# Kernel tuning notes

Hardware: AMD Instinct MI355X
Metric: run time of the kernel (lower is better)

## Reference

```python
import jax, jax.numpy as jnp
import numpy as np

# --- model hyperparams (match init_kwargs) ---
N_DIM = 200      # n_dim == nfeat == nhidden (Linear(200,200) hardcoded in source)
NHID = 200
NLAYERS = 8
ALPHA = 0.1
LAMDA = 0.5
B, L = 20, 100   # dialogues x uniform dialogue length
N = B * L        # 2000 utterances per modality -> 3N = 6000 graph nodes
A_DIM, V_DIM, L_DIM, NSPK = 300, 342, 1024, 2


def _linear_params(key, fin, fout):
    s = 1.0 / np.sqrt(fin)
    k1, k2 = jax.random.split(key)
    W = jax.random.uniform(k1, (fin, fout), jnp.float32, -s, s)
    b = jax.random.uniform(k2, (fout,), jnp.float32, -s, s)
    return W, b


def setup_inputs() -> dict:
    key = jax.random.key(0)
    ks = jax.random.split(key, 12)
    a = jax.random.normal(ks[0], (N, A_DIM), jnp.float32)
    v = jax.random.normal(ks[1], (N, V_DIM), jnp.float32)
    l = jax.random.normal(ks[2], (N, L_DIM), jnp.float32)
    qmask = jax.random.uniform(ks[3], (L, B, NSPK), dtype=jnp.float32)
    # dense normalized adjacency over the 3N-node multimodal graph
    adj = jax.random.uniform(ks[4], (3 * N, 3 * N), dtype=jnp.float32) / (3.0 * N)
    Wa, ba = _linear_params(ks[5], A_DIM, N_DIM)
    Wv, bv = _linear_params(ks[6], V_DIM, N_DIM)
    Wl, bl = _linear_params(ks[7], L_DIM, N_DIM)
    spk_emb = jax.random.normal(ks[8], (NSPK, N_DIM), jnp.float32)
    W0, b0 = _linear_params(ks[9], N_DIM, NHID)
    s = 1.0 / np.sqrt(NHID)
    # variant=True -> conv weight is [2*nhidden, nhidden]
    convW = jax.random.uniform(ks[10], (NLAYERS, 2 * NHID, NHID), jnp.float32, -s, s)
    return dict(a=a, v=v, l=l, qmask=qmask, adj=adj,
                Wa=Wa, ba=ba, Wv=Wv, bv=bv, Wl=Wl, bl=bl,
                spk_emb=spk_emb, W0=W0, b0=b0, convW=convW, dia_len=L)


def reference(a, v, l, qmask, adj, Wa, ba, Wv, bv, Wl, bl, spk_emb, W0, b0, convW, dia_len):
    # modality projections
    a = a @ Wa + ba                                   # [N, n_dim]
    v = v @ Wv + bv
    l = l @ Wl + bl
    # qmask: [L, B, n_spk] seq-first -> concat per dialogue (uniform lengths)
    qcat = jnp.transpose(qmask[:dia_len], (1, 0, 2)).reshape(-1, qmask.shape[-1])  # [N, n_spk]
    spk_idx = jnp.argmax(qcat, axis=-1)
    l = l + spk_emb[spk_idx]                          # use_speaker, 'l' in modals
    # big multimodal graph: stack modalities along node axis
    x = jnp.concatenate([a, v, l], axis=0)            # [3N, n_dim]
    # GCNII_lyc (eval mode: dropout identity)
    h0 = jax.nn.relu(x @ W0 + b0)                     # [3N, nhidden]
    thetas = jnp.log(LAMDA / jnp.arange(1, NLAYERS + 1, dtype=jnp.float32) + 1.0)

    def layer(h, wt):
        W, theta = wt
        hi = adj @ h                                  # spmm (dense here)
        support = jnp.concatenate([hi, h0], axis=1)   # variant=True
        r = (1.0 - ALPHA) * hi + ALPHA * h0
        h_new = jax.nn.relu(theta * (support @ W) + (1.0 - theta) * r)
        return h_new, None

    h, _ = jax.lax.scan(layer, h0, (convW, thetas))
    feat = jnp.concatenate([x, h], axis=1)            # use_residue -> [3N, n_dim+nhidden]
    n = a.shape[0]
    # split modality chunks back and fuse on feature axis -> [N, 3*(n_dim+nhidden)]
    return jnp.concatenate([feat[:n], feat[n:2 * n], feat[2 * n:3 * n]], axis=-1)
```

## Files before the change

### kernel.cpp

```cpp
#include <hip/hip_runtime.h>
#include <math.h>

typedef unsigned short u16;
typedef unsigned int u32;
typedef __bf16 bf8_t __attribute__((ext_vector_type(8)));
typedef float f4_t __attribute__((ext_vector_type(4)));
typedef u16 us8_t __attribute__((ext_vector_type(8)));
typedef u16 us4_t __attribute__((ext_vector_type(4)));

#define LDC 224
#define NROWS 6016
#define PLANE (NROWS*LDC)

__device__ __forceinline__ float b2f(u16 x){
  union{u32 u; float f;} c; c.u = ((u32)x)<<16; return c.f;
}
__device__ __forceinline__ u16 f2b(float f){
  union{u32 u; float f;} c; c.f = f;
  u32 b = c.u;
  return (u16)((b + 0x7FFFu + ((b>>16)&1u)) >> 16);
}
__device__ __forceinline__ u16 ldcvt(const void* p, size_t i, int f){
  return f ? f2b(((const float*)p)[i]) : ((const u16*)p)[i];
}
__device__ __forceinline__ void gl16(const u16* g, u16* l){
  __builtin_amdgcn_global_load_lds((const __attribute__((address_space(1))) void*)g,
                                   (__attribute__((address_space(3))) void*)l, 16, 0, 0);
}

__global__ void detect_kernel(const u16* __restrict__ adj, int* __restrict__ flag)
{
  int l = threadIdx.x;
  u16 u = adj[2*l];
  int ex = (u >> 7) & 0xFF;
  bool ok = ((u >> 15) == 0) && (ex >= 0x30) && (ex <= 0x72);
  unsigned long long m = __ballot(ok);
  if (l == 0) flag[0] = (__popcll(m) < 32) ? 1 : 0;
}

#define PB_MISC 5320
#define PB_XPAD 5333
#define PB_AP   5347
#define PB_VP   7907
#define PB_CONV 10979
__global__ void prep_kernel(const int* __restrict__ flag,
                            const void* __restrict__ adj, u16* __restrict__ adj_bf,
                            const void* __restrict__ Wa, const void* __restrict__ Wv,
                            const void* __restrict__ Wl, const void* __restrict__ W0,
                            const void* __restrict__ convW, const void* __restrict__ qmask,
                            const void* __restrict__ a_in, const void* __restrict__ v_in,
                            const void* __restrict__ spkemb_in,
                            const void* __restrict__ ba, const void* __restrict__ bv,
                            const void* __restrict__ bl, const void* __restrict__ b0,
                            u16* __restrict__ WaT, u16* __restrict__ WvT, u16* __restrict__ WlT,
                            u16* __restrict__ W0T, u16* __restrict__ WtT, u16* __restrict__ WbT,
                            int* __restrict__ spk, u16* __restrict__ x_bf,
                            u16* __restrict__ a_p, u16* __restrict__ v_p,
                            u16* __restrict__ spkem, u16* __restrict__ b_all)
{
  const int f = flag[0];
  const int bid = blockIdx.x;
  const int tid = threadIdx.x;

  if (bid < PB_MISC){
    u32 e = (u32)bid*256u + (u32)tid;
    const void* src; u16* dst; u32 K, kpad; u32 soff = 0;
    if (e < 71680u){ src=Wa; dst=WaT; K=300; kpad=320; }
    else if (e < 157696u){ e -= 71680u;  src=Wv; dst=WvT; K=342; kpad=384; }
    else if (e < 387072u){ e -= 157696u; src=Wl; dst=WlT; K=1024; kpad=1024; }
    else if (e < 444416u){ e -= 387072u; src=W0; dst=W0T; K=200; kpad=256; }
    else if (e < 903168u){ e -= 444416u; u32 i = e/57344u; e -= i*57344u;
                           src=convW; soff=i*80000u;          dst=WtT + i*57344; K=200; kpad=256; }
    else {                 e -= 903168u; u32 i = e/57344u; e -= i*57344u;
                           src=convW; soff=i*80000u + 40000u; dst=WbT + i*57344; K=200; kpad=256; }
    u32 k = e / 224u, n = e - k*224u;
    u16 val = 0;
    if (k < K && n < 200u) val = ldcvt(src, (size_t)soff + (size_t)k*200u + n, f);
    dst[(size_t)n*kpad + k] = val;
    return;
  }
  if (bid < PB_XPAD){
    int e = (bid - PB_MISC)*256 + tid;
    if (e < 2000){
      int b = e/100, t = e - b*100;
      size_t base = ((size_t)t*20 + b)*2;
      bool one;
      if (f) one = ((const float*)qmask)[base+1] > ((const float*)qmask)[base];
      else   one = b2f(((const u16*)qmask)[base+1]) > b2f(((const u16*)qmask)[base]);
      spk[e] = one ? 1 : 0;
    } else if (e < 2400){
      spkem[e-2000] = ldcvt(spkemb_in, e-2000, f);
    } else if (e < 3200){
      int j = e - 2400; int which = j/200, idx = j - which*200;
      const void* src = (which==0)?ba:(which==1)?bv:(which==2)?bl:b0;
      b_all[j] = ldcvt(src, idx, f);
    }
    return;
  }
  if (bid < PB_AP){
    int e = (bid - PB_XPAD)*256 + tid;
    if (e < 16*LDC) x_bf[(size_t)6000*LDC + e] = 0;
    return;
  }
  if (bid < PB_VP){
    u32 e = (u32)(bid - PB_AP)*256u + (u32)tid;
    u32 row = e / 320u, k = e - row*320u;
    a_p[e] = (row < 2000u && k < 300u) ? ldcvt(a_in, (size_t)row*300u + k, f) : (u16)0;
    return;
  }
  if (bid < PB_CONV){
    u32 e = (u32)(bid - PB_VP)*256u + (u32)tid;
    u32 row = e / 384u, k = e - row*384u;
    v_p[e] = (row < 2000u && k < 342u) ? ldcvt(v_in, (size_t)row*342u + k, f) : (u16)0;
    return;
  }
  {
    if (!adj_bf) return;
    u32 t = (u32)(bid - PB_CONV)*256u + (u32)tid;
    #pragma unroll
    for (int it=0; it<4; ++it){
      u32 idx = t + (u32)it*1131008u;
      u32 row = idx / 752u;
      int k8  = (int)(idx - row*752u) * 8;
      us8_t vv;
      if (row < 6000u){
        if (f){
          const float* src = (const float*)adj + (size_t)row*6000;
          if (k8 + 8 <= 6000){
            f4_t x0 = *(const f4_t*)(src + k8);
            f4_t x1 = *(const f4_t*)(src + k8 + 4);
            #pragma unroll
            for (int j=0;j<4;j++){ vv[j] = f2b(x0[j]); vv[4+j] = f2b(x1[j]); }
          } else {
            #pragma unroll
            for (int j=0;j<8;j++){ int k=k8+j; vv[j] = (k<6000) ? f2b(src[k]) : (u16)0; }
          }
        } else {
          const u16* src = (const u16*)adj + (size_t)row*6000;
          if (k8 + 8 <= 6000){
            vv = *(const us8_t*)(src + k8);
          } else {
            #pragma unroll
            for (int j=0;j<8;j++){ int k=k8+j; vv[j] = (k<6000) ? src[k] : (u16)0; }
          }
        }
      } else {
        #pragma unroll
        for (int j=0;j<8;j++) vv[j] = 0;
      }
      *(us8_t*)(adj_bf + (size_t)row*6016 + k8) = vv;
    }
  }
}

template<int WR>
__global__ __launch_bounds__(256, 2)
void gemm_kernel(int dynA, const int* __restrict__ flag, const u16* __restrict__ a_sel,
                 const void* __restrict__ A1, int lda1, int kv1, int kg1, int ks1, const u16* __restrict__ B1, int ldb1,
                 int Mv, int Mout, int spp, int emode,
                 const u16* __restrict__ bias, const u16* __restrict__ spk_e, const int* __restrict__ spk_idx,
                 u16* __restrict__ part_base,
                 u16* __restrict__ outN, u16* __restrict__ outT)
{
  __shared__ u16 ldsA[2][WR*32*64];
  __shared__ u16 ldsB[2][224*64];
  const int tid = threadIdx.x;
  const int l = tid & 63;
  const int w = tid >> 6;
  const int wrow = w >> 1, wcol = w & 1;
  const int row0 = blockIdx.x * (WR*32);
  const int lq = l >> 4, lr = l & 15;

  const u16* A16 = (const u16*)A1;
  const float* A32 = (const float*)A1;
  int af32 = 0, lda = lda1, kv = kv1, kg = kg1, Mvl = Mv;
  if (dynA){
    int fd = flag[0];
    if (dynA == 1){
      af32 = fd;
    } else {
      if (fd){ A16 = a_sel; lda = 6016; kv = 6016; kg = 6016; Mvl = 6016; }
    }
  }

  f4_t acc[WR][7];
  #pragma unroll
  for (int i=0;i<WR;i++)
    #pragma unroll
    for (int j=0;j<7;j++){ f4_t z = {0.f,0.f,0.f,0.f}; acc[i][j] = z; }

  int sb = blockIdx.y * spp, se = sb + spp;
  if (se > ks1) se = ks1;

  auto stageA = [&](int p, int k0){
    const u16* abase = A16 + k0;
    #pragma unroll
    for (int i=0;i<WR;i++){
      int c = (i<<8) + tid;
      int m = c >> 3, k8p = c & 7;
      int k8 = k8p ^ (m & 7);
      gl16(abase + (size_t)(row0+m)*lda + (k8<<3), &ldsA[p][c<<3]);
    }
  };
  auto stageB = [&](int p, int k0){
    const u16* bbase = B1 + k0;
    #pragma unroll
    for (int i=0;i<7;i++){
      int c = (i<<8) + tid;
      int n = c >> 3, k8p = c & 7;
      int k8 = k8p ^ (n & 7);
      gl16(bbase + (size_t)n*ldb1 + (k8<<3), &ldsB[p][c<<3]);
    }
  };
  auto computeT = [&](int p){
    #pragma unroll
    for (int h=0; h<2; ++h){
      bf8_t af[WR], bfr[7];
      int kc = lq + (h<<2);
      #pragma unroll
      for (int rt=0;rt<WR;rt++){
        int m = wrow*(16*WR) + rt*16 + lr;
        af[rt] = *(const bf8_t*)(&ldsA[p][(m<<6) + ((kc ^ (m&7))<<3)]);
      }
      #pragma unroll
      for (int ct=0;ct<7;ct++){
        int n = wcol*112 + ct*16 + lr;
        bfr[ct] = *(const bf8_t*)(&ldsB[p][(n<<6) + ((kc ^ (n&7))<<3)]);
      }
      #pragma unroll
      for (int rt=0;rt<WR;rt++)
        #pragma unroll
        for (int ct=0;ct<7;ct++)
          acc[rt][ct] = __builtin_amdgcn_mfma_f32_16x16x32_bf16(af[rt], bfr[ct], acc[rt][ct], 0,0,0);
    }
  };

  bool pipe = (!af32) && ((lda & 7) == 0) && (row0 + WR*32 <= Mvl)
              && (se > sb) && (se*64 <= kg);

  if (pipe){
    stageA(0, sb<<6); stageB(0, sb<<6);
    int p = 0;
    #pragma unroll 1
    for (int s = sb; s < se; ++s){
      if (s + 1 < se){
        stageA(p^1, (s+1)<<6); stageB(p^1, (s+1)<<6);
        if (WR == 2) asm volatile("s_waitcnt vmcnt(9)" ::: "memory");
        else         asm volatile("s_waitcnt vmcnt(8)" ::: "memory");
      } else {
        asm volatile("s_waitcnt vmcnt(0)" ::: "memory");
      }
      __builtin_amdgcn_s_barrier();
      computeT(p);
      __builtin_amdgcn_s_barrier();
      p ^= 1;
    }
  } else {
    #pragma unroll 1
    for (int s = sb; s < se; ++s){
      int k0 = s << 6;
      __syncthreads();
      bool alignedA = ((lda & 7) == 0) && (row0 + WR*32 <= Mvl);
      bool gldsA = (!af32) && alignedA && (k0 + 64 <= kg);
      if (gldsA){
        stageA(0, k0);
      } else if (af32 && alignedA && (k0 + 64 <= kv)){
        const float* ap = A32 + (size_t)row0*lda + k0;
        #pragma unroll
        for (int i=0;i<WR;i++){
          int c = (i<<8) + tid;
          int m = c >> 3, k8 = c & 7;
          f4_t x0 = *(const f4_t*)(ap + (size_t)m*lda + (k8<<3));
          f4_t x1 = *(const f4_t*)(ap + (size_t)m*lda + (k8<<3) + 4);
          us8_t vv;
          #pragma unroll
          for (int j=0;j<4;j++){ vv[j] = f2b(x0[j]); vv[4+j] = f2b(x1[j]); }
          *(us8_t*)(&ldsA[0][(m<<6) + ((k8 ^ (m&7))<<3)]) = vv;
        }
      } else {
        #pragma unroll
        for (int i=0;i<WR;i++){
          int c = (i<<8) + tid;
          int m = c >> 3, k8 = c & 7;
          int gr = row0 + m; if (gr > Mvl-1) gr = Mvl-1;
          us8_t vv;
          #pragma unroll
          for (int j=0;j<8;j++){
            int kk = k0 + (k8<<3) + j;
            u16 t = 0;
            if (kk < kv){
              if (af32) t = f2b(A32[(size_t)gr*lda + kk]);
              else      t = A16[(size_t)gr*lda + kk];
            }
            vv[j] = t;
          }
          *(us8_t*)(&ldsA[0][(m<<6) + ((k8 ^ (m&7))<<3)]) = vv;
        }
      }
      stageB(0, k0);
      __syncthreads();
      computeT(0);
    }
  }

  #pragma unroll
  for (int rt=0;rt<WR;rt++){
    int r_base = row0 + wrow*(16*WR) + rt*16 + lq*4;
    #pragma unroll
    for (int ct=0;ct<7;ct++){
      int c = wcol*112 + ct*16 + lr;
      f4_t a4 = acc[rt][ct];
      if (emode == 0){
        u16* dst = part_base + (size_t)blockIdx.y * PLANE;
        #pragma unroll
        for (int r=0;r<4;r++) dst[(size_t)(r_base+r)*LDC + c] = f2b(a4[r]);
      } else if (emode == 1){
        float bval = (c < 200) ? b2f(bias[c]) : 0.f;
        #pragma unroll
        for (int r=0;r<4;r++){
          int R = r_base + r;
          if (R < Mout){
            float vv = a4[r] + bval;
            if (spk_e && c < 200) vv += b2f(spk_e[spk_idx[R]*200 + c]);
            outN[(size_t)R*LDC + c] = f2b(vv);
          }
        }
      } else {
        float bval = (c < 200) ? b2f(bias[c]) : 0.f;
        us4_t p4;
        #pragma unroll
        for (int r=0;r<4;r++){
          int R = r_base + r;
          float vv = a4[r] + bval; if (vv < 0.f) vv = 0.f;
          u16 q = f2b(vv);
          outN[(size_t)R*LDC + c] = q;
          p4[r] = q;
        }
        *(us4_t*)(&outT[(size_t)c*NROWS + r_base]) = p4;
      }
    }
  }
}

__global__ __launch_bounds__(256, 2)
void layer_kernel(const u16* __restrict__ part, int nsk,
                  const u16* __restrict__ h0_bf,
                  const u16* __restrict__ Bt, const u16* __restrict__ Bb,
                  float theta, u16* __restrict__ outT)
{
  __shared__ u16 ldsHI[32*256];
  __shared__ u16 ldsH0[32*256];
  __shared__ u16 ldsB[2][224*64];
  const int tid = threadIdx.x;
  const int l = tid & 63;
  const int w = tid >> 6;
  const int wrow = w >> 1, wcol = w & 1;
  const int row0 = blockIdx.x * 32;
  const int lq = l >> 4, lr = l & 15;

  #pragma unroll
  for (int rr=0; rr<4; ++rr){
    int c = rr*256 + tid;
    int m = c >> 5, ch = c & 31;
    us8_t o;
    if (ch < 28){
      float s[8];
      #pragma unroll
      for (int j=0;j<8;j++) s[j] = 0.f;
      size_t base = (size_t)(row0+m)*LDC + (ch<<3);
      for (int p=0;p<nsk;p++){
        us8_t vv = *(const us8_t*)(part + (size_t)p*PLANE + base);
        #pragma unroll
        for (int j=0;j<8;j++) s[j] += b2f(vv[j]);
      }
      #pragma unroll
      for (int j=0;j<8;j++) o[j] = f2b(s[j]);
    } else {
      #pragma unroll
      for (int j=0;j<8;j++) o[j] = 0;
    }
    *(us8_t*)(&ldsHI[(m<<8) + ((ch ^ (m&7))<<3)]) = o;
    int sch = ch ^ (m&7);
    gl16(h0_bf + (size_t)(row0+m)*LDC + (sch<<3), &ldsH0[c<<3]);
  }

  auto stageB = [&](int p, int t){
    const u16* Bp = (t>>2) ? Bb : Bt;
    const u16* bbase = Bp + ((t&3)<<6);
    #pragma unroll
    for (int i=0;i<7;i++){
      int c = (i<<8) + tid;
      int n = c >> 3, k8p = c & 7;
      int k8 = k8p ^ (n & 7);
      gl16(bbase + (size_t)n*256 + (k8<<3), &ldsB[p][c<<3]);
    }
  };

  f4_t acc[7];
  #pragma unroll
  for (int j=0;j<7;j++){ f4_t z = {0.f,0.f,0.f,0.f}; acc[j] = z; }

  stageB(0, 0);
  __syncthreads();
  int p = 0;
  #pragma unroll 1
  for (int t = 0; t < 8; ++t){
    if (t < 7){
      stageB(p^1, t+1);
      asm volatile("s_waitcnt vmcnt(7)" ::: "memory");
    } else {
      asm volatile("s_waitcnt vmcnt(0)" ::: "memory");
    }
    __builtin_amdgcn_s_barrier();
    const u16* Alds = (t>>2) ? &ldsH0[0] : &ldsHI[0];
    int sloc = t & 3;
    #pragma unroll
    for (int h=0; h<2; ++h){
      int kc = lq + (h<<2);
      int m = wrow*16 + lr;
      bf8_t af = *(const bf8_t*)(&Alds[(m<<8) + (((sloc<<3) | (kc ^ (m&7)))<<3)]);
      bf8_t bfr[7];
      #pragma unroll
      for (int ct=0;ct<7;ct++){
        int n = wcol*112 + ct*16 + lr;
        bfr[ct] = *(const bf8_t*)(&ldsB[p][(n<<6) + ((kc ^ (n&7))<<3)]);
      }
      #pragma unroll
      for (int ct=0;ct<7;ct++)
        acc[ct] = __builtin_amdgcn_mfma_f32_16x16x32_bf16(af, bfr[ct], acc[ct], 0,0,0);
    }
    __builtin_amdgcn_s_barrier();
    p ^= 1;
  }

  int r_base = row0 + wrow*16 + lq*4;
  #pragma unroll
  for (int ct=0;ct<7;ct++){
    int c = wcol*112 + ct*16 + lr;
    int cc8 = c >> 3, ce = c & 7;
    us4_t p4;
    #pragma unroll
    for (int r=0;r<4;r++){
      int mr = wrow*16 + lq*4 + r;
      int ix = (mr<<8) + ((cc8 ^ (mr&7))<<3) + ce;
      float rrv = 0.9f*b2f(ldsHI[ix]) + 0.1f*b2f(ldsH0[ix]);
      float vv = theta*acc[ct][r] + (1.f - theta)*rrv;
      if (vv < 0.f) vv = 0.f;
      p4[r] = f2b(vv);
    }
    *(us4_t*)(&outT[(size_t)c*NROWS + r_base]) = p4;
  }
}

__device__ __forceinline__ u16 sent(u16 t, u16 snan, u16 sbig){
  u16 mag = t & 0x7FFF;
  if (mag >= 0x7F80) return snan;
  if (mag >= 0x4480) return sbig;
  return t;
}
__global__ void out_kernel(const int* __restrict__ flag,
                           const u16* __restrict__ x_bf, const u16* __restrict__ hT,
                           void* __restrict__ outp)
{
  __shared__ u16 tile[64*216];
  const int of32 = flag[0];
  u16* o16 = (u16*)outp;
  float* o32 = (float*)outp;
  const int tid = threadIdx.x;
  const int n0 = blockIdx.x*64;
  const int m = blockIdx.y;
  for (int cc = tid; cc < 1600; cc += 256){
    int r = cc/25, c8 = cc - r*25;
    int n = n0 + r;
    int rr = n < 2000 ? n : 1999;
    us8_t vv = *(const us8_t*)(x_bf + ((size_t)(m*2000 + rr))*LDC + c8*8);
    #pragma unroll
    for (int j=0;j<8;j++) vv[j] = sent(vv[j], 0x46EA, 0x46DB);
    if (n < 2000){
      size_t off = (size_t)n*1200 + m*400 + c8*8;
      if (!of32) *(us8_t*)(o16 + off) = vv;
      else {
        f4_t lo, hi;
        #pragma unroll
        for (int j=0;j<4;j++){ lo[j] = b2f(vv[j]); hi[j] = b2f(vv[4+j]); }
        *(f4_t*)(o32 + off) = lo; *(f4_t*)(o32 + off + 4) = hi;
      }
    }
  }
  for (int cc = tid; cc < 1600; cc += 256){
    int c = cc >> 3, ng = cc & 7;
    int nb = n0 + ng*8;
    if (nb > 1992) nb = 1992;
    us8_t vv = *(const us8_t*)(hT + (size_t)c*NROWS + m*2000 + nb);
    #pragma unroll
    for (int j=0;j<8;j++) tile[(ng*8+j)*216 + c] = sent(vv[j], 0x469C, 0x468C);
  }
  __syncthreads();
  for (int cc = tid; cc < 1600; cc += 256){
    int r = cc/25, c8 = cc - r*25;
    int n = n0 + r;
    if (n < 2000){
      us8_t vv = *(const us8_t*)(&tile[r*216 + c8*8]);
      size_t off = (size_t)n*1200 + m*400 + 200 + c8*8;
      if (!of32) *(us8_t*)(o16 + off) = vv;
      else {
        f4_t lo, hi;
        #pragma unroll
        for (int j=0;j<4;j++){ lo[j] = b2f(vv[j]); hi[j] = b2f(vv[4+j]); }
        *(f4_t*)(o32 + off) = lo; *(f4_t*)(o32 + off + 4) = hi;
      }
    }
  }
}

extern "C" void kernel_launch(void* const* d_in, const int* in_sizes, int n_in,
                              void* d_out, int out_size, void* d_ws, size_t ws_size,
                              hipStream_t stream)
{
  const void* a     = d_in[0];
  const void* v     = d_in[1];
  const void* l     = d_in[2];
  const void* qmask = d_in[3];
  const void* adj   = d_in[4];
  const void* Wa    = d_in[5];
  const void* ba    = d_in[6];
  const void* Wv    = d_in[7];
  const void* bv    = d_in[8];
  const void* Wl    = d_in[9];
  const void* bl    = d_in[10];
  const void* spk_emb = d_in[11];
  const void* W0    = d_in[12];
  const void* b0    = d_in[13];
  const void* convW = d_in[14];

  int cfg = (ws_size >= (size_t)125*1024*1024) ? 2
          : (ws_size >= (size_t)48*1024*1024) ? 1 : 0;
  const int SK = (cfg >= 1) ? 5 : 2;
  const int SPP = (94 + SK - 1) / SK;

  char* ws = (char*)d_ws;
  size_t off = 0;
  auto alloc = [&](size_t bytes)->char*{
    char* p = ws + off; off = (off + bytes + 255) & ~(size_t)255; return p;
  };
  int*  flag  = (int*) alloc(256);
  u16*  x_bf  = (u16*) alloc((size_t)PLANE*2);
  u16*  h0_bf = (u16*) alloc((size_t)PLANE*2);
  u16*  hT    = (u16*) alloc((size_t)PLANE*2);
  u16*  a_p   = (u16*) alloc((size_t)2048*320*2);
  u16*  v_p   = (u16*) alloc((size_t)2048*384*2);
  u16* WaT = (u16*)alloc(224*320*2);
  u16* WvT = (u16*)alloc(224*384*2);
  u16* WlT = (u16*)alloc(224*1024*2);
  u16* W0T = (u16*)alloc(224*256*2);
  u16* WtT = (u16*)alloc((size_t)8*224*256*2);
  u16* WbT = (u16*)alloc((size_t)8*224*256*2);
  int* spk = (int*)alloc(2000*4);
  u16* spkem = (u16*)alloc(400*2);
  u16* b_all = (u16*)alloc(800*2);
  u16* part = (u16*)alloc((size_t)SK*PLANE*2);
  u16* adj_bf = (cfg == 2) ? (u16*)alloc((size_t)6016*6016*2) : nullptr;

  detect_kernel<<<1,64,0,stream>>>((const u16*)adj, flag);

  prep_kernel<<<dim3((cfg==2) ? 15397 : 10979),256,0,stream>>>(flag, adj, adj_bf,
      Wa,Wv,Wl,W0,convW,qmask, a,v,spk_emb, ba,bv,bl,b0,
      WaT,WvT,WlT,W0T,WtT,WbT, spk, x_bf, a_p,v_p, spkem, b_all);

  gemm_kernel<1><<<dim3(64,1),256,0,stream>>>(0, nullptr, nullptr,
      a_p,320,320,320,5, WaT,320,
      2048,2000, 5, 1, b_all, nullptr, nullptr,
      nullptr, x_bf, nullptr);
  gemm_kernel<1><<<dim3(64,1),256,0,stream>>>(0, nullptr, nullptr,
      v_p,384,384,384,6, WvT,384,
      2048,2000, 6, 1, b_all+200, nullptr, nullptr,
      nullptr, x_bf + (size_t)2000*LDC, nullptr);
  gemm_kernel<1><<<dim3(64,1),256,0,stream>>>(1, flag, nullptr,
      l,1024,1024,1024,16, WlT,1024,
      2000,2000, 16, 1, b_all+400, spkem, spk,
      nullptr, x_bf + (size_t)4000*LDC, nullptr);

  gemm_kernel<1><<<dim3(188,1),256,0,stream>>>(0, nullptr, nullptr,
      x_bf,LDC,LDC,256,4, W0T,256,
      NROWS,NROWS, 4, 2, b_all+600, nullptr, nullptr,
      nullptr, h0_bf, hT);

  for (int i=0;i<8;i++){
    float theta = logf(0.5f/(float)(i+1) + 1.0f);
    if (cfg == 2)
      gemm_kernel<2><<<dim3(94,SK),256,0,stream>>>(3, flag, adj_bf,
          adj,6000,6000,6000,94, hT,NROWS,
          6000,0, SPP, 0, nullptr, nullptr, nullptr,
          part, nullptr, nullptr);
    else
      gemm_kernel<2><<<dim3(94,SK),256,0,stream>>>(1, flag, nullptr,
          adj,6000,6000,6000,94, hT,NROWS,
          6000,0, SPP, 0, nullptr, nullptr, nullptr,
          part, nullptr, nullptr);
    layer_kernel<<<dim3(188),256,0,stream>>>(part, SK, h0_bf,
        WtT + (size_t)i*57344, WbT + (size_t)i*57344, theta, hT);
  }

  out_kernel<<<dim3(32,3),256,0,stream>>>(flag, x_bf, hT, (void*)d_out);
}
```

Baseline: 669.1 us.

## Add 128-row 512-thread spmm kernel, batch adj conversion loads, coalesce layer output

Adds a dedicated spmm kernel for the adjacency-times-h product that uses 128-row tiles with 512 threads (8 waves), so each staged h tile is reused across more adjacency rows and fewer row-blocks are launched. The adjacency fp32-to-bf16 conversion now issues all four loads before converting, to raise memory-level parallelism. The layer kernel's transposed output is staged through LDS and written as 16-byte row segments instead of scattered 4-element stores. Occupancy drops to one block per CU for the spmm kernel and the generic gemm loses its dynA==3 path.

New measurement: 705.1 us. +5.4%, slower.

```diff
diff --git a/kernel.cpp b/kernel.cpp
--- a/kernel.cpp
+++ b/kernel.cpp
@@ -116,39 +116,48 @@
   }
   {
     if (!adj_bf) return;
-    u32 t = (u32)(bid - PB_CONV)*256u + (u32)tid;
+    u32 t0 = (u32)(bid - PB_CONV)*256u + (u32)tid;
+    u32 rowv[4]; int k8v[4]; int kind[4];
+    f4_t xa[4], xb[4]; us8_t ua[4];
     #pragma unroll
     for (int it=0; it<4; ++it){
-      u32 idx = t + (u32)it*1131008u;
+      u32 idx = t0 + (u32)it*1131008u;
       u32 row = idx / 752u;
       int k8  = (int)(idx - row*752u) * 8;
+      rowv[it] = row; k8v[it] = k8;
+      if (row < 6000u){
+        if (k8 + 8 <= 6000){
+          kind[it] = 0;
+          if (f){
+            const float* src = (const float*)adj + (size_t)row*6000 + k8;
+            xa[it] = *(const f4_t*)(src);
+            xb[it] = *(const f4_t*)(src + 4);
+          } else {
+            ua[it] = *(const us8_t*)((const u16*)adj + (size_t)row*6000 + k8);
+          }
+        } else kind[it] = 1;
+      } else kind[it] = 2;
+    }
+    #pragma unroll
+    for (int it=0; it<4; ++it){
       us8_t vv;
-      if (row < 6000u){
+      if (kind[it] == 0){
         if (f){
-          const float* src = (const float*)adj + (size_t)row*6000;
-          if (k8 + 8 <= 6000){
-            f4_t x0 = *(const f4_t*)(src + k8);
-            f4_t x1 = *(const f4_t*)(src + k8 + 4);
-            #pragma unroll
-            for (int j=0;j<4;j++){ vv[j] = f2b(x0[j]); vv[4+j] = f2b(x1[j]); }
-          } else {
-            #pragma unroll
-            for (int j=0;j<8;j++){ int k=k8+j; vv[j] = (k<6000) ? f2b(src[k]) : (u16)0; }
-          }
-        } else {
-          const u16* src = (const u16*)adj + (size_t)row*6000;
-          if (k8 + 8 <= 6000){
-            vv = *(const us8_t*)(src + k8);
-          } else {
-            #pragma unroll
-            for (int j=0;j<8;j++){ int k=k8+j; vv[j] = (k<6000) ? src[k] : (u16)0; }
-          }
+          #pragma unroll
+          for (int j=0;j<4;j++){ vv[j] = f2b(xa[it][j]); vv[4+j] = f2b(xb[it][j]); }
+        } else vv = ua[it];
+      } else if (kind[it] == 1){
+        int k8 = k8v[it];
+        #pragma unroll
+        for (int j=0;j<8;j++){
+          int k = k8 + j;
+          vv[j] = (k < 6000) ? ldcvt(adj, (size_t)rowv[it]*6000 + k, f) : (u16)0;
         }
       } else {
         #pragma unroll
         for (int j=0;j<8;j++) vv[j] = 0;
       }
-      *(us8_t*)(adj_bf + (size_t)row*6016 + k8) = vv;
+      *(us8_t*)(adj_bf + (size_t)rowv[it]*6016 + k8v[it]) = vv;
     }
   }
 }
@@ -176,11 +185,7 @@
   int af32 = 0, lda = lda1, kv = kv1, kg = kg1, Mvl = Mv;
   if (dynA){
     int fd = flag[0];
-    if (dynA == 1){
-      af32 = fd;
-    } else {
-      if (fd){ A16 = a_sel; lda = 6016; kv = 6016; kg = 6016; Mvl = 6016; }
-    }
+    af32 = fd;
   }
 
   f4_t acc[WR][7];
@@ -342,6 +347,140 @@
   }
 }
 
+__global__ __launch_bounds__(512, 1)
+void spmm_kernel(const int* __restrict__ flag, const void* __restrict__ adjv,
+                 const u16* __restrict__ adj_bf, const u16* __restrict__ hT,
+                 int spp, u16* __restrict__ part_base)
+{
+  __shared__ u16 ldsA[2][128*64];
+  __shared__ u16 ldsB[2][224*64];
+  const int tid = threadIdx.x;
+  const int l = tid & 63;
+  const int w = tid >> 6;
+  const int wrow = w >> 1, wcol = w & 1;
+  const int row0 = blockIdx.x * 128;
+  const int lq = l >> 4, lr = l & 15;
+
+  const int fd = flag[0];
+  const u16* A16; int lda, kv, kg, Mvl;
+  if (fd){ A16 = adj_bf; lda = 6016; kv = 6016; kg = 6016; Mvl = 6016; }
+  else   { A16 = (const u16*)adjv; lda = 6000; kv = 6000; kg = 6000; Mvl = 6000; }
+
+  f4_t acc[2][7];
+  #pragma unroll
+  for (int i=0;i<2;i++)
+    #pragma unroll
+    for (int j=0;j<7;j++){ f4_t z = {0.f,0.f,0.f,0.f}; acc[i][j] = z; }
+
+  int sb = blockIdx.y * spp, se = sb + spp;
+  if (se > 94) se = 94;
+
+  auto stageA = [&](int p, int k0){
+    const u16* abase = A16 + k0;
+    #pragma unroll
+    for (int i=0;i<2;i++){
+      int c = (i<<9) + tid;
+      int m = c >> 3, k8p = c & 7;
+      int k8 = k8p ^ (m & 7);
+      gl16(abase + (size_t)(row0+m)*lda + (k8<<3), &ldsA[p][c<<3]);
+    }
+  };
+  auto stageB = [&](int p, int k0){
+    const u16* bbase = hT + k0;
+    #pragma unroll
+    for (int i=0;i<3;i++){
+      int c = (i<<9) + tid;
+      int n = c >> 3, k8p = c & 7;
+      int k8 = k8p ^ (n & 7);
+      gl16(bbase + (size_t)n*NROWS + (k8<<3), &ldsB[p][c<<3]);
+    }
+    if (tid < 256){
+      int c = 1536 + tid;
+      int n = c >> 3, k8p = c & 7;
+      int k8 = k8p ^ (n & 7);
+      gl16(bbase + (size_t)n*NROWS + (k8<<3), &ldsB[p][c<<3]);
+    }
+  };
+  auto compute = [&](int p){
+    #pragma unroll
+    for (int h=0; h<2; ++h){
+      bf8_t af[2], bfr[7];
+      int kc = lq + (h<<2);
+      #pragma unroll
+      for (int rt=0;rt<2;rt++){
+        int m = wrow*32 + rt*16 + lr;
+        af[rt] = *(const bf8_t*)(&ldsA[p][(m<<6) + ((kc ^ (m&7))<<3)]);
+      }
+      #pragma unroll
+      for (int ct=0;ct<7;ct++){
+        int n = wcol*112 + ct*16 + lr;
+        bfr[ct] = *(const bf8_t*)(&ldsB[p][(n<<6) + ((kc ^ (n&7))<<3)]);
+      }
+      #pragma unroll
+      for (int rt=0;rt<2;rt++)
+        #pragma unroll
+        for (int ct=0;ct<7;ct++)
+          acc[rt][ct] = __builtin_amdgcn_mfma_f32_16x16x32_bf16(af[rt], bfr[ct], acc[rt][ct], 0,0,0);
+    }
+  };
+
+  bool pipe = (row0 + 128 <= Mvl) && (se > sb) && (se*64 <= kg);
+
+  if (pipe){
+    stageA(0, sb<<6); stageB(0, sb<<6);
+    int p = 0;
+    #pragma unroll 1
+    for (int s = sb; s < se; ++s){
+      if (s + 1 < se){
+        stageA(p^1, (s+1)<<6); stageB(p^1, (s+1)<<6);
+        if (tid < 256) asm volatile("s_waitcnt vmcnt(6)" ::: "memory");
+        else           asm volatile("s_waitcnt vmcnt(5)" ::: "memory");
+      } else {
+        asm volatile("s_waitcnt vmcnt(0)" ::: "memory");
+      }
+      __builtin_amdgcn_s_barrier();
+      compute(p);
+      __builtin_amdgcn_s_barrier();
+      p ^= 1;
+    }
+  } else {
+    #pragma unroll 1
+    for (int s = sb; s < se; ++s){
+      int k0 = s << 6;
+      __syncthreads();
+      #pragma unroll
+      for (int i=0;i<2;i++){
+        int c = (i<<9) + tid;
+        int m = c >> 3, k8 = c & 7;
+        int gr = row0 + m; if (gr > Mvl-1) gr = Mvl-1;
+        us8_t vv;
+        #pragma unroll
+        for (int j=0;j<8;j++){
+          int kk = k0 + (k8<<3) + j;
+          vv[j] = (kk < kv) ? A16[(size_t)gr*lda + kk] : (u16)0;
+        }
+        *(us8_t*)(&ldsA[0][(m<<6) + ((k8 ^ (m&7))<<3)]) = vv;
+      }
+      stageB(0, k0);
+      __syncthreads();
+      compute(0);
+    }
+  }
+
+  u16* dst = part_base + (size_t)blockIdx.y * PLANE;
+  #pragma unroll
+  for (int rt=0;rt<2;rt++){
+    int r_base = row0 + wrow*32 + rt*16 + lq*4;
+    #pragma unroll
+    for (int ct=0;ct<7;ct++){
+      int c = wcol*112 + ct*16 + lr;
+      f4_t a4 = acc[rt][ct];
+      #pragma unroll
+      for (int r=0;r<4;r++) dst[(size_t)(r_base+r)*LDC + c] = f2b(a4[r]);
+    }
+  }
+}
+
 __global__ __launch_bounds__(256, 2)
 void layer_kernel(const u16* __restrict__ part, int nsk,
                   const u16* __restrict__ h0_bf,
@@ -433,22 +572,30 @@
     p ^= 1;
   }
 
-  int r_base = row0 + wrow*16 + lq*4;
-  #pragma unroll
-  for (int ct=0;ct<7;ct++){
-    int c = wcol*112 + ct*16 + lr;
-    int cc8 = c >> 3, ce = c & 7;
-    us4_t p4;
-    #pragma unroll
-    for (int r=0;r<4;r++){
-      int mr = wrow*16 + lq*4 + r;
-      int ix = (mr<<8) + ((cc8 ^ (mr&7))<<3) + ce;
-      float rrv = 0.9f*b2f(ldsHI[ix]) + 0.1f*b2f(ldsH0[ix]);
-      float vv = theta*acc[ct][r] + (1.f - theta)*rrv;
-      if (vv < 0.f) vv = 0.f;
-      p4[r] = f2b(vv);
-    }
-    *(us4_t*)(&outT[(size_t)c*NROWS + r_base]) = p4;
+  u16* ldsT = &ldsB[0][0];
+  __syncthreads();
+  {
+    int mr0 = wrow*16 + lq*4;
+    #pragma unroll
+    for (int ct=0;ct<7;ct++){
+      int c = wcol*112 + ct*16 + lr;
+      int cc8 = c >> 3, ce = c & 7;
+      #pragma unroll
+      for (int r=0;r<4;r++){
+        int mr = mr0 + r;
+        int ix = (mr<<8) + ((cc8 ^ (mr&7))<<3) + ce;
+        float rrv = 0.9f*b2f(ldsHI[ix]) + 0.1f*b2f(ldsH0[ix]);
+        float vv = theta*acc[ct][r] + (1.f - theta)*rrv;
+        if (vv < 0.f) vv = 0.f;
+        ldsT[c*32 + mr] = f2b(vv);
+      }
+    }
+  }
+  __syncthreads();
+  for (int cc = tid; cc < 896; cc += 256){
+    int c = cc >> 2, g = cc & 3;
+    us8_t vv = *(const us8_t*)(&ldsT[c*32 + (g<<3)]);
+    *(us8_t*)(&outT[(size_t)c*NROWS + row0 + (g<<3)]) = vv;
   }
 }
 
@@ -588,10 +735,7 @@
   for (int i=0;i<8;i++){
     float theta = logf(0.5f/(float)(i+1) + 1.0f);
     if (cfg == 2)
-      gemm_kernel<2><<<dim3(94,SK),256,0,stream>>>(3, flag, adj_bf,
-          adj,6000,6000,6000,94, hT,NROWS,
-          6000,0, SPP, 0, nullptr, nullptr, nullptr,
-          part, nullptr, nullptr);
+      spmm_kernel<<<dim3(47,SK),512,0,stream>>>(flag, adj, adj_bf, hT, SPP, part);
     else
       gemm_kernel<2><<<dim3(94,SK),256,0,stream>>>(1, flag, nullptr,
           adj,6000,6000,6000,94, hT,NROWS,
```
